# Performance work log

Measured on AMD Instinct MI355X. Metric: run time of the kernel, lower is better.

The kernel has to match this reference:

```python
import jax, jax.numpy as jnp
import numpy as np

C = 512
NUM_HEADS = 8
HEAD_DIM = 64
GROUPS = 32
EPS = 1e-5


def setup_inputs() -> dict:
    key = jax.random.key(0)
    ks = jax.random.split(key, 7)
    x = jax.random.normal(ks[0], (2, C, 64, 64), dtype=jnp.float32)
    norm_w = jnp.ones((C,), jnp.float32)
    norm_b = jnp.zeros((C,), jnp.float32)
    s1 = 1.0 / np.sqrt(C)
    qkv_w = jax.random.uniform(ks[1], (3 * C, C), jnp.float32, -s1, s1)
    qkv_b = jax.random.uniform(ks[2], (3 * C,), jnp.float32, -s1, s1)
    proj_w = jax.random.uniform(ks[3], (C, C), jnp.float32, -s1, s1)
    proj_b = jax.random.uniform(ks[4], (C,), jnp.float32, -s1, s1)
    return {"x": x, "norm_w": norm_w, "norm_b": norm_b,
            "qkv_w": qkv_w, "qkv_b": qkv_b,
            "proj_w": proj_w, "proj_b": proj_b}


def reference(x, norm_w, norm_b, qkv_w, qkv_b, proj_w, proj_b):
    b, c, h, w = x.shape
    n = h * w
    x_flat = x.reshape(b, c, n)
    # GroupNorm(32, C): stats over (channels-in-group, spatial)
    xg = x_flat.reshape(b, GROUPS, c // GROUPS, n)
    mean = xg.mean(axis=(2, 3), keepdims=True)
    var = xg.var(axis=(2, 3), keepdims=True)
    hn = ((xg - mean) * jax.lax.rsqrt(var + EPS)).reshape(b, c, n)
    hn = hn * norm_w[None, :, None] + norm_b[None, :, None]
    # 1x1 conv QKV = matmul over channel dim
    qkv = jnp.einsum('oc,bcn->bon', qkv_w, hn) + qkv_b[None, :, None]
    q, k, v = jnp.split(qkv, 3, axis=1)
    q = q.reshape(b, NUM_HEADS, HEAD_DIM, n)
    k = k.reshape(b, NUM_HEADS, HEAD_DIM, n)
    v = v.reshape(b, NUM_HEADS, HEAD_DIM, n)
    scale = HEAD_DIM ** (-0.5)
    attn = jnp.einsum('bhdn,bhdm->bhnm', q, k) * scale  # [b,H,N,N]
    attn = jax.nn.softmax(attn, axis=-1)
    out = jnp.einsum('bhnm,bhdm->bhdn', attn, v).reshape(b, c, n)
    out = jnp.einsum('oc,bcn->bon', proj_w, out) + proj_b[None, :, None]
    return (x_flat + out).reshape(b, c, h, w)
```

## Files before the change

### kernel.cpp

```cpp
#include <hip/hip_runtime.h>
#include <hip/hip_bf16.h>
#include <math.h>

#define BATCH 2
#define CCH   512
#define NSP   4096
#define NHEAD 8
#define HDIM  64
#define NGRP  32
#define CPG   16
#define EPSV  1e-5f
#define NSPLIT 2
#define MTN   (NSP / NSPLIT / 64)
#define SMSCALE 0.1803368801111204f

typedef __attribute__((ext_vector_type(8))) short short8;
typedef __attribute__((ext_vector_type(4))) short short4v;
typedef __attribute__((ext_vector_type(4))) float f32x4;
typedef __hip_bfloat16 bf16;

static __device__ __forceinline__ unsigned pk2(float a, float b) {
    return ((__float_as_uint(a) + 0x8000u) >> 16) |
           ((__float_as_uint(b) + 0x8000u) & 0xFFFF0000u);
}
static __device__ __forceinline__ unsigned pk1(float a) {
    return (__float_as_uint(a) + 0x8000u) >> 16;
}
static __device__ __forceinline__ float upk(unsigned u) {
    unsigned v = u << 16;
    return __uint_as_float(v);
}
static __device__ __forceinline__ float fexp2(float x) {
    return __builtin_amdgcn_exp2f(x);
}
static __device__ __forceinline__ void gload16(const bf16* g, bf16* l) {
    __builtin_amdgcn_global_load_lds(
        (const __attribute__((address_space(1))) unsigned*)g,
        (__attribute__((address_space(3))) unsigned*)l, 16, 0, 0);
}

__global__ __launch_bounds__(256) void prep0(const float* __restrict__ x,
                                             const float* __restrict__ qkvw,
                                             const float* __restrict__ pw,
                                             float* __restrict__ sbuf,
                                             bf16* __restrict__ wq, bf16* __restrict__ wp) {
    if (blockIdx.x < 1024) {
        const int bg = blockIdx.x >> 4, sub = blockIdx.x & 15;
        const float4* p = (const float4*)(x + (size_t)bg * (CPG * NSP)) +
                          (size_t)sub * (CPG * NSP / 4 / 16);
        float s = 0.f, ss = 0.f;
#pragma unroll
        for (int it = 0; it < 4; it++) {
            float4 v = p[it * 256 + threadIdx.x];
            s  += v.x + v.y + v.z + v.w;
            ss += v.x * v.x + v.y * v.y + v.z * v.z + v.w * v.w;
        }
        for (int o = 32; o > 0; o >>= 1) {
            s  += __shfl_down(s, o);
            ss += __shfl_down(ss, o);
        }
        __shared__ float shs[4], shss[4];
        const int wid = threadIdx.x >> 6, lane = threadIdx.x & 63;
        if (lane == 0) { shs[wid] = s; shss[wid] = ss; }
        __syncthreads();
        if (threadIdx.x == 0) {
            s  = shs[0] + shs[1] + shs[2] + shs[3];
            ss = shss[0] + shss[1] + shss[2] + shss[3];
            sbuf[bg * 16 + sub]        = s;
            sbuf[1024 + bg * 16 + sub] = ss;
        }
    } else {
        const int i = (blockIdx.x - 1024) * 256 + threadIdx.x;
        const int NQ = 1536 * 512 / 4;
        float4 v; bf16* dst; int di;
        if (i < NQ) { v = ((const float4*)qkvw)[i]; dst = wq; di = i; }
        else        { v = ((const float4*)pw)[i - NQ]; dst = wp; di = i - NQ; }
        uint2 o = {pk2(v.x, v.y), pk2(v.z, v.w)};
        *(uint2*)(dst + (size_t)di * 4) = o;
    }
}

__global__ __launch_bounds__(256) void gn_apply_t(const float* __restrict__ x,
                                                  const float* __restrict__ sbuf,
                                                  const float* __restrict__ nw,
                                                  const float* __restrict__ nb,
                                                  bf16* __restrict__ hnt) {
    __shared__ float Ls[64][68];
    const int b  = blockIdx.z;
    const int c0 = blockIdx.y * 64;
    const int n0 = blockIdx.x * 64;
    const int t  = threadIdx.x;
    const int cl = t >> 4, n4 = (t & 15) * 4;
    const float invn = 1.f / (float)(CPG * NSP);
#pragma unroll
    for (int ph = 0; ph < 4; ph++) {
        const int c  = c0 + ph * 16 + cl;
        const int bg = b * NGRP + (c >> 4);
        float s = 0.f, ss = 0.f;
#pragma unroll
        for (int i = 0; i < 16; i++) {
            s  += sbuf[bg * 16 + i];
            ss += sbuf[1024 + bg * 16 + i];
        }
        const float mu = s * invn;
        const float rs = rsqrtf(ss * invn - mu * mu + EPSV);
        const float sw = nw[c] * rs;
        const float sb = nb[c] - mu * sw;
        float4 v = *(const float4*)&x[((size_t)b * CCH + c) * NSP + n0 + n4];
        float4 o;
        o.x = v.x * sw + sb; o.y = v.y * sw + sb;
        o.z = v.z * sw + sb; o.w = v.w * sw + sb;
        *(float4*)&Ls[ph * 16 + cl][n4] = o;
    }
    __syncthreads();
#pragma unroll
    for (int ph = 0; ph < 2; ph++) {
        const int task = ph * 256 + t;
        const int nl = task & 63, cc = (task >> 6) * 8;
        uint4 o;
        o.x = pk2(Ls[cc + 0][nl], Ls[cc + 1][nl]);
        o.y = pk2(Ls[cc + 2][nl], Ls[cc + 3][nl]);
        o.z = pk2(Ls[cc + 4][nl], Ls[cc + 5][nl]);
        o.w = pk2(Ls[cc + 6][nl], Ls[cc + 7][nl]);
        *(uint4*)&hnt[((size_t)b * NSP + n0 + nl) * CCH + c0 + cc] = o;
    }
}

#define GEMM_STAGE(CUR)                                         \
    gload16(aSrc0, &As[CUR][(wave * 16) * 32]);                 \
    gload16(aSrc1, &As[CUR][(64 + wave * 16) * 32]);            \
    gload16(bSrc0, &Bs[CUR][(wave * 16) * 32]);                 \
    gload16(bSrc1, &Bs[CUR][(64 + wave * 16) * 32]);            \
    aSrc0 += 32; aSrc1 += 32; bSrc0 += 32; bSrc1 += 32;

#define GEMM_MAIN(Wptr, Xptr)                                                            \
    __shared__ __align__(16) bf16 As[2][128 * 32];                                       \
    __shared__ __align__(16) bf16 Bs[2][128 * 32];                                       \
    const int t = threadIdx.x, wave = t >> 6, lane = t & 63;                             \
    const int quad = lane >> 4, l15 = lane & 15;                                         \
    const int srow = lane >> 2, scol = (lane & 3) * 8;                                   \
    const int b   = blockIdx.z;                                                          \
    const int wm = wave >> 1, wn = wave & 1;                                             \
    const int m0w = blockIdx.y * 128 + wm * 64;                                          \
    const int n0w = blockIdx.x * 128 + wn * 64;                                          \
    const bf16* aSrc0 = Wptr + (size_t)(blockIdx.y * 128 + wave * 16 + srow) * 512 + scol; \
    const bf16* aSrc1 = aSrc0 + (size_t)64 * 512;                                        \
    const bf16* bSrc0 = Xptr + ((size_t)b * NSP + blockIdx.x * 128 + wave * 16 + srow) * 512 + scol; \
    const bf16* bSrc1 = bSrc0 + (size_t)64 * 512;                                        \
    f32x4 acc[4][4];                                                                     \
    _Pragma("unroll")                                                                    \
    for (int i = 0; i < 4; i++)                                                          \
        _Pragma("unroll")                                                                \
        for (int j = 0; j < 4; j++) acc[i][j] = (f32x4){0.f, 0.f, 0.f, 0.f};             \
    GEMM_STAGE(0)                                                                        \
    __syncthreads();                                                                     \
    _Pragma("unroll")                                                                    \
    for (int ks = 0; ks < 16; ks++) {                                                    \
        const int cur = ks & 1;                                                          \
        if (ks < 15) { GEMM_STAGE(cur ^ 1) }                                             \
        short8 af[4], bfr[4];                                                            \
        _Pragma("unroll")                                                                \
        for (int mf = 0; mf < 4; mf++)                                                   \
            af[mf] = *(const short8*)&As[cur][(wm * 64 + mf * 16 + l15) * 32 + quad * 8]; \
        _Pragma("unroll")                                                                \
        for (int nf = 0; nf < 4; nf++)                                                   \
            bfr[nf] = *(const short8*)&Bs[cur][(wn * 64 + nf * 16 + l15) * 32 + quad * 8]; \
        _Pragma("unroll")                                                                \
        for (int mf = 0; mf < 4; mf++)                                                   \
            _Pragma("unroll")                                                            \
            for (int nf = 0; nf < 4; nf++)                                               \
                acc[mf][nf] = __builtin_amdgcn_mfma_f32_16x16x32_bf16(af[mf], bfr[nf],   \
                                                                      acc[mf][nf], 0, 0, 0); \
        __syncthreads();                                                                 \
    }

__global__ __launch_bounds__(256) void gemm_qkv(const bf16* __restrict__ Wb,
                                                const bf16* __restrict__ Xt,
                                                const float* __restrict__ bias,
                                                bf16* __restrict__ qt, bf16* __restrict__ kt,
                                                bf16* __restrict__ vt) {
    GEMM_MAIN(Wb, Xt)

    const int sec = m0w >> 9, h = (m0w >> 6) & 7, bh = b * NHEAD + h;
    const float sm = (sec == 0) ? SMSCALE : 1.0f;
    float bi[4][4];
#pragma unroll
    for (int mf = 0; mf < 4; mf++)
#pragma unroll
        for (int r = 0; r < 4; r++) bi[mf][r] = bias[m0w + mf * 16 + quad * 4 + r];

    if (sec < 2) {
        bf16* dst = (sec == 0) ? qt : kt;
#pragma unroll
        for (int mf = 0; mf < 4; mf++)
#pragma unroll
            for (int nf = 0; nf < 4; nf++) {
                const int n = n0w + nf * 16 + l15;
                float v0 = (acc[mf][nf][0] + bi[mf][0]) * sm;
                float v1 = (acc[mf][nf][1] + bi[mf][1]) * sm;
                float v2 = (acc[mf][nf][2] + bi[mf][2]) * sm;
                float v3 = (acc[mf][nf][3] + bi[mf][3]) * sm;
                uint2 o = {pk2(v0, v1), pk2(v2, v3)};
                *(uint2*)(dst + ((size_t)bh * NSP + n) * HDIM + mf * 16 + quad * 4) = o;
            }
    } else {
#pragma unroll
        for (int mf = 0; mf < 4; mf++)
#pragma unroll
            for (int nf = 0; nf < 4; nf++)
#pragma unroll
                for (int r = 0; r < 4; r++) {
                    const float v = acc[mf][nf][r] + bi[mf][r];
                    const int n = n0w + nf * 16 + l15;
                    const int d = mf * 16 + quad * 4 + r;
                    unsigned u = pk1(v);
                    vt[((size_t)bh * HDIM + d) * NSP + n] = *(bf16*)&u;
                }
    }
}

__global__ __launch_bounds__(256) void gemm_proj(const bf16* __restrict__ Wb,
                                                 const bf16* __restrict__ Xt,
                                                 const float* __restrict__ bias,
                                                 const float* __restrict__ resid,
                                                 float* __restrict__ out) {
    GEMM_MAIN(Wb, Xt)

    float bi[4][4];
#pragma unroll
    for (int mf = 0; mf < 4; mf++)
#pragma unroll
        for (int r = 0; r < 4; r++) bi[mf][r] = bias[m0w + mf * 16 + quad * 4 + r];
#pragma unroll
    for (int mf = 0; mf < 4; mf++)
#pragma unroll
        for (int nf = 0; nf < 4; nf++)
#pragma unroll
            for (int r = 0; r < 4; r++) {
                const int m = m0w + mf * 16 + quad * 4 + r;
                const int n = n0w + nf * 16 + l15;
                const size_t idx = ((size_t)b * CCH + m) * NSP + n;
                out[idx] = acc[mf][nf][r] + bi[mf][r] + resid[idx];
            }
}

__global__ __launch_bounds__(256, 2) void attn10(const bf16* __restrict__ qt,
                                                 const bf16* __restrict__ kt,
                                                 const bf16* __restrict__ vt,
                                                 bf16* __restrict__ opart,
                                                 float* __restrict__ lpart) {
    __shared__ __align__(16) bf16 Ks[64][68];
    __shared__ __align__(16) bf16 Vs[64][68];
    const int t = threadIdx.x, wave = t >> 6, lane = t & 63;
    const int quad = lane >> 4, l15 = lane & 15;
    const int blk = blockIdx.x;
    const int xcd = blk & 7, slot = blk >> 3;
    const int qtile = slot & 15;
    const int grp = xcd + 8 * (slot >> 4);
    const int spl = grp & 1, bh = grp >> 1;
    const int b = bh >> 3, h = bh & 7;
    const int qb  = qtile * 256 + wave * 64;
    const int kb0 = spl * (NSP / NSPLIT);

    const bf16* Qb = qt + (size_t)bh * NSP * HDIM;

    const int trow = t >> 3;
    const int tcol = (t & 7) * 8;
    const bf16* kSrcA = kt + (size_t)bh * NSP * HDIM + (size_t)(kb0 + trow) * HDIM + tcol;
    const bf16* kSrcB = kSrcA + 32 * HDIM;
    const bf16* vSrcA = vt + (size_t)bh * HDIM * NSP + (size_t)trow * NSP + kb0 + tcol;
    const bf16* vSrcB = vSrcA + (size_t)32 * NSP;
    bf16* kDstA = &Ks[trow][tcol];
    bf16* kDstB = &Ks[32 + trow][tcol];
    bf16* vDstA = &Vs[trow][tcol];
    bf16* vDstB = &Vs[32 + trow][tcol];

    short8 qf[4][2];
#pragma unroll
    for (int qs = 0; qs < 4; qs++)
#pragma unroll
        for (int c = 0; c < 2; c++)
            qf[qs][c] = *(const short8*)(Qb + (size_t)(qb + qs * 16 + l15) * HDIM + c * 32 + quad * 8);

    short8 onesf;
    {
        const short one = (short)0x3F80;
        short8 o1 = {one, one, one, one, one, one, one, one};
        short8 zz = {0, 0, 0, 0, 0, 0, 0, 0};
        onesf = (l15 == 0) ? o1 : zz;
    }

    f32x4 o[4][4], ol[4];
#pragma unroll
    for (int qs = 0; qs < 4; qs++) {
        ol[qs] = (f32x4){0.f, 0.f, 0.f, 0.f};
#pragma unroll
        for (int ds = 0; ds < 4; ds++) o[qs][ds] = (f32x4){0.f, 0.f, 0.f, 0.f};
    }

    uint4 rKA = *(const uint4*)kSrcA; kSrcA += 64 * HDIM;
    uint4 rKB = *(const uint4*)kSrcB; kSrcB += 64 * HDIM;
    uint4 rVA = *(const uint4*)vSrcA; vSrcA += 64;
    uint4 rVB = *(const uint4*)vSrcB; vSrcB += 64;

    for (int mt = 0; mt < MTN; mt++) {
        __syncthreads();
        *(uint4*)kDstA = rKA;
        *(uint4*)kDstB = rKB;
        *(uint4*)vDstA = rVA;
        *(uint4*)vDstB = rVB;
        __syncthreads();

        rKA = *(const uint4*)kSrcA; kSrcA += 64 * HDIM;
        rKB = *(const uint4*)kSrcB; kSrcB += 64 * HDIM;
        rVA = *(const uint4*)vSrcA; vSrcA += 64;
        rVB = *(const uint4*)vSrcB; vSrcB += 64;

        short8 kf[4][2], vf[4][2];
#pragma unroll
        for (int ms = 0; ms < 4; ms++)
#pragma unroll
            for (int c = 0; c < 2; c++)
                kf[ms][c] = *(const short8*)&Ks[ms * 16 + l15][c * 32 + quad * 8];
#pragma unroll
        for (int ds = 0; ds < 4; ds++)
#pragma unroll
            for (int c = 0; c < 2; c++)
                vf[ds][c] = *(const short8*)&Vs[ds * 16 + l15][c * 32 + quad * 8];

#pragma unroll
        for (int qs = 0; qs < 4; qs++) {
            f32x4 s[4];
            __builtin_amdgcn_s_setprio(1);
#pragma unroll
            for (int ms = 0; ms < 4; ms++) {
                f32x4 a = (f32x4){0.f, 0.f, 0.f, 0.f};
                a = __builtin_amdgcn_mfma_f32_16x16x32_bf16(kf[ms][0], qf[qs][0], a, 0, 0, 0);
                a = __builtin_amdgcn_mfma_f32_16x16x32_bf16(kf[ms][1], qf[qs][1], a, 0, 0, 0);
                s[ms] = a;
            }
            __builtin_amdgcn_s_setprio(0);

            unsigned rr[4][2];
#pragma unroll
            for (int ms = 0; ms < 4; ms++) {
                float e0 = fexp2(s[ms][0]);
                float e1 = fexp2(s[ms][1]);
                float e2 = fexp2(s[ms][2]);
                float e3 = fexp2(s[ms][3]);
                asm("v_cvt_pk_bf16_f32 %0, %1, %2" : "=v"(rr[ms][0]) : "v"(e0), "v"(e1));
                asm("v_cvt_pk_bf16_f32 %0, %1, %2" : "=v"(rr[ms][1]) : "v"(e2), "v"(e3));
            }
#pragma unroll
            for (int j = 0; j < 2; j++) {
                asm("v_permlane32_swap_b32 %0, %1" : "+v"(rr[0][j]), "+v"(rr[1][j]));
                asm("v_permlane32_swap_b32 %0, %1" : "+v"(rr[2][j]), "+v"(rr[3][j]));
            }
#pragma unroll
            for (int j = 0; j < 2; j++) {
                asm("v_permlane16_swap_b32 %0, %1" : "+v"(rr[0][j]), "+v"(rr[1][j]));
                asm("v_permlane16_swap_b32 %0, %1" : "+v"(rr[2][j]), "+v"(rr[3][j]));
            }
            short8 pf0, pf1;
            {
                unsigned* p0 = (unsigned*)&pf0;
                p0[0] = rr[0][0]; p0[1] = rr[0][1]; p0[2] = rr[1][0]; p0[3] = rr[1][1];
                unsigned* p1 = (unsigned*)&pf1;
                p1[0] = rr[2][0]; p1[1] = rr[2][1]; p1[2] = rr[3][0]; p1[3] = rr[3][1];
            }

            __builtin_amdgcn_s_setprio(1);
#pragma unroll
            for (int ds = 0; ds < 4; ds++) {
                f32x4 a = o[qs][ds];
                a = __builtin_amdgcn_mfma_f32_16x16x32_bf16(pf0, vf[ds][0], a, 0, 0, 0);
                a = __builtin_amdgcn_mfma_f32_16x16x32_bf16(pf1, vf[ds][1], a, 0, 0, 0);
                o[qs][ds] = a;
            }
            {
                f32x4 a = ol[qs];
                a = __builtin_amdgcn_mfma_f32_16x16x32_bf16(pf0, onesf, a, 0, 0, 0);
                a = __builtin_amdgcn_mfma_f32_16x16x32_bf16(pf1, onesf, a, 0, 0, 0);
                ol[qs] = a;
            }
            __builtin_amdgcn_s_setprio(0);
        }
    }

#pragma unroll
    for (int qs = 0; qs < 4; qs++) {
#pragma unroll
        for (int ds = 0; ds < 4; ds++)
#pragma unroll
            for (int r = 0; r < 4; r++) {
                const int q = qb + qs * 16 + quad * 4 + r;
                unsigned u = pk1(o[qs][ds][r]);
                opart[((size_t)(spl * BATCH + b) * NSP + q) * CCH + h * 64 + ds * 16 + l15] =
                    *(bf16*)&u;
            }
        if (l15 == 0) {
#pragma unroll
            for (int r = 0; r < 4; r++) {
                const int q = qb + qs * 16 + quad * 4 + r;
                lpart[(((size_t)spl * BATCH + b) * NHEAD + h) * NSP + q] = ol[qs][r];
            }
        }
    }
}

__global__ __launch_bounds__(256) void attn_combine(const bf16* __restrict__ opart,
                                                    const float* __restrict__ lpart,
                                                    bf16* __restrict__ att_t) {
    const int idx = blockIdx.x * 256 + threadIdx.x;
    const int c8 = (idx & 63) * 8;
    const int n  = (idx >> 6) & 4095;
    const int b  = idx >> 18;
    const int h  = c8 >> 6;
    float l = 0.f;
#pragma unroll
    for (int s = 0; s < NSPLIT; s++)
        l += lpart[(((size_t)s * BATCH + b) * NHEAD + h) * NSP + n];
    const float inv = 1.f / l;
    float acc[8] = {};
#pragma unroll
    for (int s = 0; s < NSPLIT; s++) {
        uint4 u = *(const uint4*)&opart[((size_t)(s * BATCH + b) * NSP + n) * CCH + c8];
        acc[0] += upk(u.x); acc[1] += upk(u.x >> 16);
        acc[2] += upk(u.y); acc[3] += upk(u.y >> 16);
        acc[4] += upk(u.z); acc[5] += upk(u.z >> 16);
        acc[6] += upk(u.w); acc[7] += upk(u.w >> 16);
    }
    uint4 o;
    o.x = pk2(acc[0] * inv, acc[1] * inv);
    o.y = pk2(acc[2] * inv, acc[3] * inv);
    o.z = pk2(acc[4] * inv, acc[5] * inv);
    o.w = pk2(acc[6] * inv, acc[7] * inv);
    *(uint4*)&att_t[((size_t)b * NSP + n) * CCH + c8] = o;
}

extern "C" void kernel_launch(void* const* d_in, const int* in_sizes, int n_in,
                              void* d_out, int out_size, void* d_ws, size_t ws_size,
                              hipStream_t stream) {
    const float* x    = (const float*)d_in[0];
    const float* nw   = (const float*)d_in[1];
    const float* nb   = (const float*)d_in[2];
    const float* qkvw = (const float*)d_in[3];
    const float* qkvb = (const float*)d_in[4];
    const float* pw   = (const float*)d_in[5];
    const float* pb   = (const float*)d_in[6];
    float* out = (float*)d_out;
    char* ws   = (char*)d_ws;

    float* sbuf = (float*)ws;
    bf16* wq  = (bf16*)(ws + (size_t)1  * 1024 * 1024);
    bf16* wp  = (bf16*)(ws + (size_t)3  * 1024 * 1024);
    bf16* hnt = (bf16*)(ws + (size_t)4  * 1024 * 1024);
    bf16* qtb = (bf16*)(ws + (size_t)12 * 1024 * 1024);
    bf16* ktb = (bf16*)(ws + (size_t)20 * 1024 * 1024);
    bf16* vtb = (bf16*)(ws + (size_t)28 * 1024 * 1024);
    bf16* opart = (bf16*)(ws + (size_t)36 * 1024 * 1024);
    float* lpart = (float*)(ws + (size_t)56 * 1024 * 1024);
    bf16* att = hnt;

    hipLaunchKernelGGL(prep0, dim3(1024 + 1024), dim3(256), 0, stream,
                       x, qkvw, pw, sbuf, wq, wp);
    hipLaunchKernelGGL(gn_apply_t, dim3(NSP / 64, CCH / 64, BATCH), dim3(256), 0, stream,
                       x, sbuf, nw, nb, hnt);
    hipLaunchKernelGGL(gemm_qkv, dim3(NSP / 128, 1536 / 128, BATCH), dim3(256), 0, stream,
                       wq, hnt, qkvb, qtb, ktb, vtb);
    hipLaunchKernelGGL(attn10, dim3(512), dim3(256), 0, stream,
                       qtb, ktb, vtb, opart, lpart);
    hipLaunchKernelGGL(attn_combine, dim3(BATCH * NSP * CCH / 8 / 256), dim3(256), 0, stream,
                       opart, lpart, att);
    hipLaunchKernelGGL(gemm_proj, dim3(NSP / 128, CCH / 128, BATCH), dim3(256), 0, stream,
                       wp, att, pb, x, out);
}
```

Measured before the change: 207.2 us.

## Double-buffer K/V shared tiles in attention kernel to halve barriers

Makes the K and V shared-memory tiles in the attention kernel double-buffered. The loop now writes the next tile into the idle buffer while computing on the current one, which needs one barrier per tile instead of two. The aim is to cut barrier stalls and overlap the LDS stores with MFMA work. In exchange, shared memory per block doubles, and the prefetch now reads one more tile past the end of each split.

```diff
diff --git a/kernel.cpp b/kernel.cpp
--- a/kernel.cpp
+++ b/kernel.cpp
@@ -249,8 +249,8 @@
                                                  const bf16* __restrict__ vt,
                                                  bf16* __restrict__ opart,
                                                  float* __restrict__ lpart) {
-    __shared__ __align__(16) bf16 Ks[64][68];
-    __shared__ __align__(16) bf16 Vs[64][68];
+    __shared__ __align__(16) bf16 Ks[2][64][68];
+    __shared__ __align__(16) bf16 Vs[2][64][68];
     const int t = threadIdx.x, wave = t >> 6, lane = t & 63;
     const int quad = lane >> 4, l15 = lane & 15;
     const int blk = blockIdx.x;
@@ -270,10 +270,6 @@
     const bf16* kSrcB = kSrcA + 32 * HDIM;
     const bf16* vSrcA = vt + (size_t)bh * HDIM * NSP + (size_t)trow * NSP + kb0 + tcol;
     const bf16* vSrcB = vSrcA + (size_t)32 * NSP;
-    bf16* kDstA = &Ks[trow][tcol];
-    bf16* kDstB = &Ks[32 + trow][tcol];
-    bf16* vDstA = &Vs[trow][tcol];
-    bf16* vDstB = &Vs[32 + trow][tcol];
 
     short8 qf[4][2];
 #pragma unroll
@@ -298,94 +294,105 @@
         for (int ds = 0; ds < 4; ds++) o[qs][ds] = (f32x4){0.f, 0.f, 0.f, 0.f};
     }
 
-    uint4 rKA = *(const uint4*)kSrcA; kSrcA += 64 * HDIM;
-    uint4 rKB = *(const uint4*)kSrcB; kSrcB += 64 * HDIM;
-    uint4 rVA = *(const uint4*)vSrcA; vSrcA += 64;
-    uint4 rVB = *(const uint4*)vSrcB; vSrcB += 64;
-
-    for (int mt = 0; mt < MTN; mt++) {
+    uint4 rKA, rKB, rVA, rVB;
+#define ATTN_LOAD()                                         \
+    rKA = *(const uint4*)kSrcA; kSrcA += 64 * HDIM;         \
+    rKB = *(const uint4*)kSrcB; kSrcB += 64 * HDIM;         \
+    rVA = *(const uint4*)vSrcA; vSrcA += 64;                \
+    rVB = *(const uint4*)vSrcB; vSrcB += 64;
+#define ATTN_STAGE(BUF)                                     \
+    *(uint4*)&Ks[BUF][trow][tcol] = rKA;                    \
+    *(uint4*)&Ks[BUF][32 + trow][tcol] = rKB;               \
+    *(uint4*)&Vs[BUF][trow][tcol] = rVA;                    \
+    *(uint4*)&Vs[BUF][32 + trow][tcol] = rVB;
+#define ATTN_COMPUTE(BUF)                                                                \
+    {                                                                                    \
+        short8 kf[4][2], vf[4][2];                                                       \
+        _Pragma("unroll")                                                                \
+        for (int ms = 0; ms < 4; ms++)                                                   \
+            _Pragma("unroll")                                                            \
+            for (int c = 0; c < 2; c++)                                                  \
+                kf[ms][c] = *(const short8*)&Ks[BUF][ms * 16 + l15][c * 32 + quad * 8];  \
+        _Pragma("unroll")                                                                \
+        for (int ds = 0; ds < 4; ds++)                                                   \
+            _Pragma("unroll")                                                            \
+            for (int c = 0; c < 2; c++)                                                  \
+                vf[ds][c] = *(const short8*)&Vs[BUF][ds * 16 + l15][c * 32 + quad * 8];  \
+        _Pragma("unroll")                                                                \
+        for (int qs = 0; qs < 4; qs++) {                                                 \
+            f32x4 s[4];                                                                  \
+            __builtin_amdgcn_s_setprio(1);                                               \
+            _Pragma("unroll")                                                            \
+            for (int ms = 0; ms < 4; ms++) {                                             \
+                f32x4 a = (f32x4){0.f, 0.f, 0.f, 0.f};                                   \
+                a = __builtin_amdgcn_mfma_f32_16x16x32_bf16(kf[ms][0], qf[qs][0], a, 0, 0, 0); \
+                a = __builtin_amdgcn_mfma_f32_16x16x32_bf16(kf[ms][1], qf[qs][1], a, 0, 0, 0); \
+                s[ms] = a;                                                               \
+            }                                                                            \
+            __builtin_amdgcn_s_setprio(0);                                               \
+            unsigned rr[4][2];                                                           \
+            _Pragma("unroll")                                                            \
+            for (int ms = 0; ms < 4; ms++) {                                             \
+                float e0 = fexp2(s[ms][0]);                                              \
+                float e1 = fexp2(s[ms][1]);                                              \
+                float e2 = fexp2(s[ms][2]);                                              \
+                float e3 = fexp2(s[ms][3]);                                              \
+                asm("v_cvt_pk_bf16_f32 %0, %1, %2" : "=v"(rr[ms][0]) : "v"(e0), "v"(e1)); \
+                asm("v_cvt_pk_bf16_f32 %0, %1, %2" : "=v"(rr[ms][1]) : "v"(e2), "v"(e3)); \
+            }                                                                            \
+            _Pragma("unroll")                                                            \
+            for (int j = 0; j < 2; j++) {                                                \
+                asm("v_permlane32_swap_b32 %0, %1" : "+v"(rr[0][j]), "+v"(rr[1][j]));    \
+                asm("v_permlane32_swap_b32 %0, %1" : "+v"(rr[2][j]), "+v"(rr[3][j]));    \
+            }                                                                            \
+            _Pragma("unroll")                                                            \
+            for (int j = 0; j < 2; j++) {                                                \
+                asm("v_permlane16_swap_b32 %0, %1" : "+v"(rr[0][j]), "+v"(rr[1][j]));    \
+                asm("v_permlane16_swap_b32 %0, %1" : "+v"(rr[2][j]), "+v"(rr[3][j]));    \
+            }                                                                            \
+            short8 pf0, pf1;                                                             \
+            {                                                                            \
+                unsigned* p0 = (unsigned*)&pf0;                                          \
+                p0[0] = rr[0][0]; p0[1] = rr[0][1]; p0[2] = rr[1][0]; p0[3] = rr[1][1];  \
+                unsigned* p1 = (unsigned*)&pf1;                                          \
+                p1[0] = rr[2][0]; p1[1] = rr[2][1]; p1[2] = rr[3][0]; p1[3] = rr[3][1];  \
+            }                                                                            \
+            __builtin_amdgcn_s_setprio(1);                                               \
+            _Pragma("unroll")                                                            \
+            for (int ds = 0; ds < 4; ds++) {                                             \
+                f32x4 a = o[qs][ds];                                                     \
+                a = __builtin_amdgcn_mfma_f32_16x16x32_bf16(pf0, vf[ds][0], a, 0, 0, 0); \
+                a = __builtin_amdgcn_mfma_f32_16x16x32_bf16(pf1, vf[ds][1], a, 0, 0, 0); \
+                o[qs][ds] = a;                                                           \
+            }                                                                            \
+            {                                                                            \
+                f32x4 a = ol[qs];                                                        \
+                a = __builtin_amdgcn_mfma_f32_16x16x32_bf16(pf0, onesf, a, 0, 0, 0);     \
+                a = __builtin_amdgcn_mfma_f32_16x16x32_bf16(pf1, onesf, a, 0, 0, 0);     \
+                ol[qs] = a;                                                              \
+            }                                                                            \
+            __builtin_amdgcn_s_setprio(0);                                               \
+        }                                                                                \
+    }
+
+    ATTN_LOAD()
+    ATTN_STAGE(0)
+    ATTN_LOAD()
+    __syncthreads();
+
+    for (int mt = 0; mt < MTN; mt += 2) {
+        ATTN_STAGE(1)
+        ATTN_LOAD()
+        ATTN_COMPUTE(0)
         __syncthreads();
-        *(uint4*)kDstA = rKA;
-        *(uint4*)kDstB = rKB;
-        *(uint4*)vDstA = rVA;
-        *(uint4*)vDstB = rVB;
+        ATTN_STAGE(0)
+        ATTN_LOAD()
+        ATTN_COMPUTE(1)
         __syncthreads();
-
-        rKA = *(const uint4*)kSrcA; kSrcA += 64 * HDIM;
-        rKB = *(const uint4*)kSrcB; kSrcB += 64 * HDIM;
-        rVA = *(const uint4*)vSrcA; vSrcA += 64;
-        rVB = *(const uint4*)vSrcB; vSrcB += 64;
-
-        short8 kf[4][2], vf[4][2];
-#pragma unroll
-        for (int ms = 0; ms < 4; ms++)
-#pragma unroll
-            for (int c = 0; c < 2; c++)
-                kf[ms][c] = *(const short8*)&Ks[ms * 16 + l15][c * 32 + quad * 8];
-#pragma unroll
-        for (int ds = 0; ds < 4; ds++)
-#pragma unroll
-            for (int c = 0; c < 2; c++)
-                vf[ds][c] = *(const short8*)&Vs[ds * 16 + l15][c * 32 + quad * 8];
-
-#pragma unroll
-        for (int qs = 0; qs < 4; qs++) {
-            f32x4 s[4];
-            __builtin_amdgcn_s_setprio(1);
-#pragma unroll
-            for (int ms = 0; ms < 4; ms++) {
-                f32x4 a = (f32x4){0.f, 0.f, 0.f, 0.f};
-                a = __builtin_amdgcn_mfma_f32_16x16x32_bf16(kf[ms][0], qf[qs][0], a, 0, 0, 0);
-                a = __builtin_amdgcn_mfma_f32_16x16x32_bf16(kf[ms][1], qf[qs][1], a, 0, 0, 0);
-                s[ms] = a;
-            }
-            __builtin_amdgcn_s_setprio(0);
-
-            unsigned rr[4][2];
-#pragma unroll
-            for (int ms = 0; ms < 4; ms++) {
-                float e0 = fexp2(s[ms][0]);
-                float e1 = fexp2(s[ms][1]);
-                float e2 = fexp2(s[ms][2]);
-                float e3 = fexp2(s[ms][3]);
-                asm("v_cvt_pk_bf16_f32 %0, %1, %2" : "=v"(rr[ms][0]) : "v"(e0), "v"(e1));
-                asm("v_cvt_pk_bf16_f32 %0, %1, %2" : "=v"(rr[ms][1]) : "v"(e2), "v"(e3));
-            }
-#pragma unroll
-            for (int j = 0; j < 2; j++) {
-                asm("v_permlane32_swap_b32 %0, %1" : "+v"(rr[0][j]), "+v"(rr[1][j]));
-                asm("v_permlane32_swap_b32 %0, %1" : "+v"(rr[2][j]), "+v"(rr[3][j]));
-            }
-#pragma unroll
-            for (int j = 0; j < 2; j++) {
-                asm("v_permlane16_swap_b32 %0, %1" : "+v"(rr[0][j]), "+v"(rr[1][j]));
-                asm("v_permlane16_swap_b32 %0, %1" : "+v"(rr[2][j]), "+v"(rr[3][j]));
-            }
-            short8 pf0, pf1;
-            {
-                unsigned* p0 = (unsigned*)&pf0;
-                p0[0] = rr[0][0]; p0[1] = rr[0][1]; p0[2] = rr[1][0]; p0[3] = rr[1][1];
-                unsigned* p1 = (unsigned*)&pf1;
-                p1[0] = rr[2][0]; p1[1] = rr[2][1]; p1[2] = rr[3][0]; p1[3] = rr[3][1];
-            }
-
-            __builtin_amdgcn_s_setprio(1);
-#pragma unroll
-            for (int ds = 0; ds < 4; ds++) {
-                f32x4 a = o[qs][ds];
-                a = __builtin_amdgcn_mfma_f32_16x16x32_bf16(pf0, vf[ds][0], a, 0, 0, 0);
-                a = __builtin_amdgcn_mfma_f32_16x16x32_bf16(pf1, vf[ds][1], a, 0, 0, 0);
-                o[qs][ds] = a;
-            }
-            {
-                f32x4 a = ol[qs];
-                a = __builtin_amdgcn_mfma_f32_16x16x32_bf16(pf0, onesf, a, 0, 0, 0);
-                a = __builtin_amdgcn_mfma_f32_16x16x32_bf16(pf1, onesf, a, 0, 0, 0);
-                ol[qs] = a;
-            }
-            __builtin_amdgcn_s_setprio(0);
-        }
-    }
+    }
+#undef ATTN_LOAD
+#undef ATTN_STAGE
+#undef ATTN_COMPUTE
 
 #pragma unroll
     for (int qs = 0; qs < 4; qs++) {
```

Measured after the change: 206.4 us. Within noise of the previous version (-0.4%).
